# Kernel tuning notes

Measured on AMD Instinct MI355X. Metric: run time of the kernel, lower is better.

## Reference

```python
import jax, jax.numpy as jnp
import numpy as np

INPUT_DIM = 32
HID_DIM = 64
TTCN_DIM = HID_DIM - 1  # 63
N, LX = 128, 512


def setup_inputs() -> dict:
    key = jax.random.key(0)
    ks = jax.random.split(key, 10)
    X_int = jax.random.normal(ks[0], (N, LX, INPUT_DIM), dtype=jnp.float32)
    mask_X = jax.random.randint(ks[1], (N, LX, 1), 0, 2).astype(jnp.float32)
    s1 = 1.0 / np.sqrt(INPUT_DIM)
    s2 = 1.0 / np.sqrt(TTCN_DIM)
    W1 = jax.random.uniform(ks[2], (INPUT_DIM, TTCN_DIM), jnp.float32, -s1, s1)
    b1 = jax.random.uniform(ks[3], (TTCN_DIM,), jnp.float32, -s1, s1)
    W2 = jax.random.uniform(ks[4], (TTCN_DIM, TTCN_DIM), jnp.float32, -s2, s2)
    b2 = jax.random.uniform(ks[5], (TTCN_DIM,), jnp.float32, -s2, s2)
    W3 = jax.random.uniform(ks[6], (TTCN_DIM, INPUT_DIM * TTCN_DIM), jnp.float32, -s2, s2)
    b3 = jax.random.uniform(ks[7], (INPUT_DIM * TTCN_DIM,), jnp.float32, -s2, s2)
    T_bias = jax.random.normal(ks[8], (1, TTCN_DIM), dtype=jnp.float32)
    return {"X_int": X_int, "mask_X": mask_X, "W1": W1, "b1": b1,
            "W2": W2, "b2": b2, "W3": W3, "b3": b3, "T_bias": T_bias}


def reference(X_int, mask_X, W1, b1, W2, b2, W3, b3, T_bias):
    n, lx, d = X_int.shape
    k = TTCN_DIM
    # 3-layer MLP filter generator: (N, Lx, D*K)
    h = jax.nn.relu(X_int @ W1 + b1)
    h = jax.nn.relu(h @ W2 + b2)
    filt = h @ W3 + b3
    # masked softmax over the time axis Lx
    filt = filt * mask_X + (1.0 - mask_X) * (-1e8)
    filt = jax.nn.softmax(filt, axis=1)  # softmax over Lx
    filt = filt.reshape(n, lx, k, d)     # (N, Lx, K, D)
    # attention-weighted pooling: sum over Lx and D
    out = jnp.einsum('nld,nlkd->nk', X_int, filt)
    return jax.nn.relu(out + T_bias)
```

## Files before the change

kernel.cpp:

```cpp
#include <hip/hip_runtime.h>
#include <hip/hip_bf16.h>


#define N_   128
#define LX_  512
#define D_   32
#define K_   63
#define C_   2016
#define LOG2E 1.44269504088896f

typedef __bf16 bf16x8 __attribute__((ext_vector_type(8)));
typedef float floatx4 __attribute__((ext_vector_type(4)));

static __device__ __forceinline__ floatx4 mfma16(bf16x8 a, bf16x8 b, floatx4 c) {
  return __builtin_amdgcn_mfma_f32_16x16x32_bf16(a, b, c, 0, 0, 0);
}

#define HC_OFF   0u
#define XMC_OFF  (8u * 1024u * 1024u)
#define W3FR_OFF (12u * 1024u * 1024u)
#define W1FR_OFF (W3FR_OFF + 258048u)
#define W2FR_OFF (W1FR_OFF + 4096u)
#define B1_OFF   (W2FR_OFF + 8192u)
#define POS_OFF  (B1_OFF + 256u)
#define CNT_OFF  (POS_OFF + 262144u)

__global__ __launch_bounds__(256) void kern_prep(
    const float* __restrict__ Mk,
    const float* __restrict__ W1, const float* __restrict__ b1,
    const float* __restrict__ W2, const float* __restrict__ b2,
    const float* __restrict__ W3, const float* __restrict__ b3,
    __bf16* __restrict__ W3fr, __bf16* __restrict__ W1fr,
    __bf16* __restrict__ W2fr, float* __restrict__ b1pad,
    int* __restrict__ pos, int* __restrict__ cnt,
    __bf16* __restrict__ Hc, __bf16* __restrict__ Xmc) {
  const int n = blockIdx.x, tid = threadIdx.x;
  __shared__ int s_cnt;

  if (tid < 64) {
    const int lane = tid;
    int running = 0;
    for (int c = 0; c < 8; ++c) {
      const int l = c * 64 + lane;
      const float mkv = Mk[n * LX_ + l];
      const unsigned long long b = __ballot(mkv > 0.5f);
      const int mypos = running + __popcll(b & ((1ull << lane) - 1ull));
      pos[n * LX_ + l] = (mkv > 0.5f) ? mypos : -1;
      running += __popcll(b);
    }
    if (lane == 0) { cnt[n] = running; s_cnt = running; }
  }
  __syncthreads();

  const int c0 = s_cnt, c1 = (c0 + 63) & ~63;
  const float4 z = {0.f, 0.f, 0.f, 0.f};
  for (int idx = tid; idx < (c1 - c0) * 12; idx += 256) {
    const int row = c0 + idx / 12, q = idx % 12;
    if (q < 8) *(float4*)(Hc  + ((size_t)(n * 512 + row)) * 64 + q * 8) = z;
    else       *(float4*)(Xmc + ((size_t)(n * 512 + row)) * 32 + (q - 8) * 8) = z;
  }

  for (int g = n * 256 + tid; g < 129024 + 2048 + 4096 + 64; g += N_ * 256) {
    if (g < 129024) {
      const int j = g & 7, quad = (g >> 3) & 3, l16 = (g >> 5) & 15, h = (g >> 9) & 1;
      const int rest = g >> 10, i = rest % 6, tile = rest / 6;
      const int c = tile * 96 + i * 16 + l16;
      const int t = h * 32 + quad * 8 + j;
      W3fr[g] = (__bf16)(((t < K_) ? W3[(size_t)t * C_ + c] : b3[c]) * LOG2E);
    } else if (g < 129024 + 2048) {
      const int g2 = g - 129024;
      const int j = g2 & 7, quad = (g2 >> 3) & 3, l16 = (g2 >> 5) & 15, i = g2 >> 9;
      const int ch = i * 16 + l16, t = quad * 8 + j;
      W1fr[g2] = (__bf16)((ch < K_) ? W1[t * K_ + ch] : 0.f);
    } else if (g < 129024 + 2048 + 4096) {
      const int g2 = g - 129024 - 2048;
      const int j = g2 & 7, quad = (g2 >> 3) & 3, l16 = (g2 >> 5) & 15, h = (g2 >> 9) & 1;
      const int i = g2 >> 10;
      const int ch = i * 16 + l16, t = h * 32 + quad * 8 + j;
      float v;
      if (t < K_) v = (ch < K_) ? W2[t * K_ + ch] : 0.f;
      else        v = (ch < K_) ? b2[ch] : 1.f;
      W2fr[g2] = (__bf16)v;
    } else {
      const int g2 = g - 129024 - 2048 - 4096;
      b1pad[g2] = (g2 < K_) ? b1[g2] : 0.f;
    }
  }
}

__global__ __launch_bounds__(256) void kern_mlp(
    const float* __restrict__ X, const __bf16* __restrict__ W1fr,
    const __bf16* __restrict__ W2fr, const float* __restrict__ b1pad,
    const int* __restrict__ pos, __bf16* __restrict__ Hc,
    __bf16* __restrict__ Xmc) {
  __shared__ float h1s[4][16][68];
  const int tid = threadIdx.x;
  const int w = tid >> 6, lane = tid & 63, quad = lane >> 4, l16 = lane & 15;

  bf16x8 b1f[4], b2f[4][2];
  float b1v[4];
#pragma unroll
  for (int i = 0; i < 4; ++i) {
    b1f[i]    = *(const bf16x8*)(W1fr + ((i * 16 + l16) * 4 + quad) * 8);
    b2f[i][0] = *(const bf16x8*)(W2fr + (((i * 2 + 0) * 16 + l16) * 4 + quad) * 8);
    b2f[i][1] = *(const bf16x8*)(W2fr + (((i * 2 + 1) * 16 + l16) * 4 + quad) * 8);
    b1v[i] = b1pad[i * 16 + l16];
  }

  const int tok0 = blockIdx.x * 64 + w * 16;
  const int n = tok0 >> 9;
  const float* xp = X + (size_t)(tok0 + l16) * D_ + quad * 8;
  const float4 xa = *(const float4*)xp;
  const float4 xb = *(const float4*)(xp + 4);
  bf16x8 a1;
  a1[0]=(__bf16)xa.x; a1[1]=(__bf16)xa.y; a1[2]=(__bf16)xa.z; a1[3]=(__bf16)xa.w;
  a1[4]=(__bf16)xb.x; a1[5]=(__bf16)xb.y; a1[6]=(__bf16)xb.z; a1[7]=(__bf16)xb.w;

  const int px = pos[tok0 + l16];
  int pr[4];
#pragma unroll
  for (int r = 0; r < 4; ++r) pr[r] = pos[tok0 + quad * 4 + r];

  if (px >= 0)
    *(bf16x8*)(Xmc + ((size_t)(n * 512 + px)) * 32 + quad * 8) = a1;

#pragma unroll
  for (int i = 0; i < 4; ++i) {
    floatx4 acc = {0.f, 0.f, 0.f, 0.f};
    acc = mfma16(a1, b1f[i], acc);
#pragma unroll
    for (int r = 0; r < 4; ++r) {
      float v = fmaxf(acc[r] + b1v[i], 0.f);
      if (i == 3 && l16 == 15) v = 1.f;
      h1s[w][quad * 4 + r][i * 16 + l16] = v;
    }
  }

  const float* hrow = &h1s[w][l16][0];
  const float4 p0 = *(const float4*)(hrow + quad * 8);
  const float4 p1 = *(const float4*)(hrow + quad * 8 + 4);
  const float4 p2 = *(const float4*)(hrow + 32 + quad * 8);
  const float4 p3 = *(const float4*)(hrow + 32 + quad * 8 + 4);
  bf16x8 a20, a21;
  a20[0]=(__bf16)p0.x; a20[1]=(__bf16)p0.y; a20[2]=(__bf16)p0.z; a20[3]=(__bf16)p0.w;
  a20[4]=(__bf16)p1.x; a20[5]=(__bf16)p1.y; a20[6]=(__bf16)p1.z; a20[7]=(__bf16)p1.w;
  a21[0]=(__bf16)p2.x; a21[1]=(__bf16)p2.y; a21[2]=(__bf16)p2.z; a21[3]=(__bf16)p2.w;
  a21[4]=(__bf16)p3.x; a21[5]=(__bf16)p3.y; a21[6]=(__bf16)p3.z; a21[7]=(__bf16)p3.w;

#pragma unroll
  for (int i = 0; i < 4; ++i) {
    floatx4 acc = {0.f, 0.f, 0.f, 0.f};
    acc = mfma16(a20, b2f[i][0], acc);
    acc = mfma16(a21, b2f[i][1], acc);
#pragma unroll
    for (int r = 0; r < 4; ++r) {
      if (pr[r] >= 0)
        Hc[((size_t)(n * 512 + pr[r])) * 64 + i * 16 + l16] =
            (__bf16)fmaxf(acc[r], 0.f);
    }
  }
}

__global__ __launch_bounds__(256) void kern_att(
    const __bf16* __restrict__ Hc, const __bf16* __restrict__ Xmc,
    const __bf16* __restrict__ W3fr, const int* __restrict__ cnt,
    const float* __restrict__ Tb, float* __restrict__ out) {
  __shared__ float redS[4][96], redO[4][96];
  __shared__ float rbuf[96];

  const int bid = blockIdx.x;
  const int idx = bid >> 3;
  const int n = (bid & 7) * 16 + idx / 21;
  const int bt = idx % 21;
  const int tid = threadIdx.x;
  const int w = tid >> 6, lane = tid & 63, quad = lane >> 4, l16 = lane & 15;

  bf16x8 bf[6][2];
#pragma unroll
  for (int i = 0; i < 6; ++i) {
    bf[i][0] = *(const bf16x8*)(W3fr + ((((bt * 6 + i) * 2 + 0) * 16 + l16) * 4 + quad) * 8);
    bf[i][1] = *(const bf16x8*)(W3fr + ((((bt * 6 + i) * 2 + 1) * 16 + l16) * 4 + quad) * 8);
  }

  const int cntn = cnt[n];
  const int iters = (cntn + 63) >> 6;
  const __bf16* Hn = Hc + ((size_t)n << 9) * 64;
  const __bf16* Xn = Xmc + ((size_t)n << 9) * 32;

  float s[6] = {0, 0, 0, 0, 0, 0}, o[6] = {0, 0, 0, 0, 0, 0};

  int lw = w * 16;
  bf16x8 a0 = *(const bf16x8*)(Hn + (size_t)(lw + l16) * 64 + quad * 8);
  bf16x8 a1 = *(const bf16x8*)(Hn + (size_t)(lw + l16) * 64 + 32 + quad * 8);
  float xl[4], xh[4];
#pragma unroll
  for (int r = 0; r < 4; ++r) {
    xl[r] = (float)Xn[(lw + quad * 4 + r) * 32 + l16];
    xh[r] = (float)Xn[(lw + quad * 4 + r) * 32 + 16 + l16];
  }

#pragma unroll 1
  for (int it = 0;;) {
    bf16x8 na0, na1;
    float nxl[4], nxh[4];
    const int nlw = lw + 64;
    if (it + 1 < iters) {
      na0 = *(const bf16x8*)(Hn + (size_t)(nlw + l16) * 64 + quad * 8);
      na1 = *(const bf16x8*)(Hn + (size_t)(nlw + l16) * 64 + 32 + quad * 8);
#pragma unroll
      for (int r = 0; r < 4; ++r) {
        nxl[r] = (float)Xn[(nlw + quad * 4 + r) * 32 + l16];
        nxh[r] = (float)Xn[(nlw + quad * 4 + r) * 32 + 16 + l16];
      }
    }

    float v[4];
#pragma unroll
    for (int r = 0; r < 4; ++r) v[r] = (lw + quad * 4 + r < cntn) ? 1.f : 0.f;

#pragma unroll
    for (int i = 0; i < 6; ++i) {
      floatx4 acc = {0.f, 0.f, 0.f, 0.f};
      acc = mfma16(a0, bf[i][0], acc);
      acc = mfma16(a1, bf[i][1], acc);
      const float* xv = (i & 1) ? xh : xl;
#pragma unroll
      for (int r = 0; r < 4; ++r) {
        const float e = __builtin_amdgcn_exp2f(acc[r]);
        s[i] = fmaf(v[r], e, s[i]);
        o[i] = fmaf(e, xv[r], o[i]);
      }
    }

    if (++it >= iters) break;
    lw = nlw;
    a0 = na0; a1 = na1;
#pragma unroll
    for (int r = 0; r < 4; ++r) { xl[r] = nxl[r]; xh[r] = nxh[r]; }
  }

#pragma unroll
  for (int i = 0; i < 6; ++i) {
    s[i] += __shfl_xor(s[i], 16);
    s[i] += __shfl_xor(s[i], 32);
    o[i] += __shfl_xor(o[i], 16);
    o[i] += __shfl_xor(o[i], 32);
  }
  if (quad == 0) {
#pragma unroll
    for (int i = 0; i < 6; ++i) {
      redS[w][i * 16 + l16] = s[i];
      redO[w][i * 16 + l16] = o[i];
    }
  }
  __syncthreads();
  if (tid < 96) {
    const float S = redS[0][tid] + redS[1][tid] + redS[2][tid] + redS[3][tid];
    const float O = redO[0][tid] + redO[1][tid] + redO[2][tid] + redO[3][tid];
    rbuf[tid] = O / S;
  }
  __syncthreads();
  if (tid < 3) {
    float acc = 0.f;
#pragma unroll
    for (int dd = 0; dd < 32; ++dd) acc += rbuf[tid * 32 + dd];
    const int k = bt * 3 + tid;
    out[n * K_ + k] = fmaxf(acc + Tb[k], 0.f);
  }
}

extern "C" void kernel_launch(void* const* d_in, const int* in_sizes, int n_in,
                              void* d_out, int out_size, void* d_ws, size_t ws_size,
                              hipStream_t stream) {
  const float* X  = (const float*)d_in[0];
  const float* Mk = (const float*)d_in[1];
  const float* W1 = (const float*)d_in[2];
  const float* b1 = (const float*)d_in[3];
  const float* W2 = (const float*)d_in[4];
  const float* b2 = (const float*)d_in[5];
  const float* W3 = (const float*)d_in[6];
  const float* b3 = (const float*)d_in[7];
  const float* Tb = (const float*)d_in[8];
  float* out = (float*)d_out;

  char* ws = (char*)d_ws;
  __bf16* Hc    = (__bf16*)(ws + HC_OFF);
  __bf16* Xmc   = (__bf16*)(ws + XMC_OFF);
  __bf16* W3fr  = (__bf16*)(ws + W3FR_OFF);
  __bf16* W1fr  = (__bf16*)(ws + W1FR_OFF);
  __bf16* W2fr  = (__bf16*)(ws + W2FR_OFF);
  float*  b1pad = (float*)(ws + B1_OFF);
  int*    pos   = (int*)(ws + POS_OFF);
  int*    cnt   = (int*)(ws + CNT_OFF);

  kern_prep<<<N_, 256, 0, stream>>>(Mk, W1, b1, W2, b2, W3, b3,
                                    W3fr, W1fr, W2fr, b1pad, pos, cnt, Hc, Xmc);
  kern_mlp<<<N_ * LX_ / 64, 256, 0, stream>>>(X, W1fr, W2fr, b1pad, pos, Hc, Xmc);
  kern_att<<<N_ * 21, 256, 0, stream>>>(Hc, Xmc, W3fr, cnt, Tb, out);
}
```

Baseline: 113.7 us.

## Store compacted X transposed in fp32 chunks and process 16-row chunks in attention

Compacted X is now stored as fp32 in a chunk-transposed layout, so the attention kernel reads it with float4 loads instead of scalar bf16 gathers. The attention loop now steps through 16-row chunks instead of 64-row iterations, which trims wasted padded work. The per-row validity mask is dropped and the padded rows' contribution to the softmax sum is subtracted afterwards. The transposed writes in the MLP kernel become strided scalar stores, and the fp32 buffer doubles the workspace traffic for X.

```diff
diff --git a/kernel.cpp b/kernel.cpp
--- a/kernel.cpp
+++ b/kernel.cpp
@@ -11,14 +11,15 @@
 
 typedef __bf16 bf16x8 __attribute__((ext_vector_type(8)));
 typedef float floatx4 __attribute__((ext_vector_type(4)));
+typedef float floatx2 __attribute__((ext_vector_type(2)));
 
 static __device__ __forceinline__ floatx4 mfma16(bf16x8 a, bf16x8 b, floatx4 c) {
   return __builtin_amdgcn_mfma_f32_16x16x32_bf16(a, b, c, 0, 0, 0);
 }
 
 #define HC_OFF   0u
-#define XMC_OFF  (8u * 1024u * 1024u)
-#define W3FR_OFF (12u * 1024u * 1024u)
+#define XT_OFF   (8u * 1024u * 1024u)
+#define W3FR_OFF (16u * 1024u * 1024u)
 #define W1FR_OFF (W3FR_OFF + 258048u)
 #define W2FR_OFF (W1FR_OFF + 4096u)
 #define B1_OFF   (W2FR_OFF + 8192u)
@@ -33,7 +34,7 @@
     __bf16* __restrict__ W3fr, __bf16* __restrict__ W1fr,
     __bf16* __restrict__ W2fr, float* __restrict__ b1pad,
     int* __restrict__ pos, int* __restrict__ cnt,
-    __bf16* __restrict__ Hc, __bf16* __restrict__ Xmc) {
+    __bf16* __restrict__ Hc, float* __restrict__ Xt) {
   const int n = blockIdx.x, tid = threadIdx.x;
   __shared__ int s_cnt;
 
@@ -54,10 +55,14 @@
 
   const int c0 = s_cnt, c1 = (c0 + 63) & ~63;
   const float4 z = {0.f, 0.f, 0.f, 0.f};
-  for (int idx = tid; idx < (c1 - c0) * 12; idx += 256) {
-    const int row = c0 + idx / 12, q = idx % 12;
-    if (q < 8) *(float4*)(Hc  + ((size_t)(n * 512 + row)) * 64 + q * 8) = z;
-    else       *(float4*)(Xmc + ((size_t)(n * 512 + row)) * 32 + (q - 8) * 8) = z;
+  for (int idx = tid; idx < (c1 - c0) * 40; idx += 256) {
+    const int row = c0 + idx / 40, q = idx % 40;
+    if (q < 8) {
+      *(float4*)(Hc + ((size_t)(n * 512 + row)) * 64 + q * 8) = z;
+    } else {
+      const int d = q - 8;
+      Xt[((size_t)(n * 32 + (row >> 4)) * 32 + d) * 16 + (row & 15)] = 0.f;
+    }
   }
 
   for (int g = n * 256 + tid; g < 129024 + 2048 + 4096 + 64; g += N_ * 256) {
@@ -92,7 +97,7 @@
     const float* __restrict__ X, const __bf16* __restrict__ W1fr,
     const __bf16* __restrict__ W2fr, const float* __restrict__ b1pad,
     const int* __restrict__ pos, __bf16* __restrict__ Hc,
-    __bf16* __restrict__ Xmc) {
+    float* __restrict__ Xt) {
   __shared__ float h1s[4][16][68];
   const int tid = threadIdx.x;
   const int w = tid >> 6, lane = tid & 63, quad = lane >> 4, l16 = lane & 15;
@@ -121,8 +126,12 @@
 #pragma unroll
   for (int r = 0; r < 4; ++r) pr[r] = pos[tok0 + quad * 4 + r];
 
-  if (px >= 0)
-    *(bf16x8*)(Xmc + ((size_t)(n * 512 + px)) * 32 + quad * 8) = a1;
+  if (px >= 0) {
+    float* xtp = Xt + ((size_t)(n * 32 + (px >> 4)) * 32 + quad * 8) * 16 + (px & 15);
+    const float vals[8] = {xa.x, xa.y, xa.z, xa.w, xb.x, xb.y, xb.z, xb.w};
+#pragma unroll
+    for (int j = 0; j < 8; ++j) xtp[j * 16] = vals[j];
+  }
 
 #pragma unroll
   for (int i = 0; i < 4; ++i) {
@@ -162,7 +171,7 @@
 }
 
 __global__ __launch_bounds__(256) void kern_att(
-    const __bf16* __restrict__ Hc, const __bf16* __restrict__ Xmc,
+    const __bf16* __restrict__ Hc, const float* __restrict__ Xt,
     const __bf16* __restrict__ W3fr, const int* __restrict__ cnt,
     const float* __restrict__ Tb, float* __restrict__ out) {
   __shared__ float redS[4][96], redO[4][96];
@@ -183,79 +192,77 @@
   }
 
   const int cntn = cnt[n];
-  const int iters = (cntn + 63) >> 6;
-  const __bf16* Hn = Hc + ((size_t)n << 9) * 64;
-  const __bf16* Xn = Xmc + ((size_t)n << 9) * 32;
-
-  float s[6] = {0, 0, 0, 0, 0, 0}, o[6] = {0, 0, 0, 0, 0, 0};
-
-  int lw = w * 16;
-  bf16x8 a0 = *(const bf16x8*)(Hn + (size_t)(lw + l16) * 64 + quad * 8);
-  bf16x8 a1 = *(const bf16x8*)(Hn + (size_t)(lw + l16) * 64 + 32 + quad * 8);
-  float xl[4], xh[4];
-#pragma unroll
-  for (int r = 0; r < 4; ++r) {
-    xl[r] = (float)Xn[(lw + quad * 4 + r) * 32 + l16];
-    xh[r] = (float)Xn[(lw + quad * 4 + r) * 32 + 16 + l16];
-  }
+  const int nch = (cntn + 15) >> 4;
+  const __bf16* Hb = Hc + ((size_t)n << 9) * 64 + (size_t)l16 * 64 + quad * 8;
+  const float*  Xb = Xt + ((size_t)n * 32) * 512 + l16 * 16 + quad * 4;
+
+  floatx2 s2[3] = {{0.f, 0.f}, {0.f, 0.f}, {0.f, 0.f}};
+  float o[6] = {0, 0, 0, 0, 0, 0};
+
+  int c = w;
+  bf16x8 a0 = *(const bf16x8*)(Hb + (size_t)c * 1024);
+  bf16x8 a1 = *(const bf16x8*)(Hb + (size_t)c * 1024 + 32);
+  float4 xl4 = *(const float4*)(Xb + c * 512);
+  float4 xh4 = *(const float4*)(Xb + c * 512 + 256);
 
 #pragma unroll 1
-  for (int it = 0;;) {
+  while (c < nch) {
+    const int cn = c + 4;
     bf16x8 na0, na1;
-    float nxl[4], nxh[4];
-    const int nlw = lw + 64;
-    if (it + 1 < iters) {
-      na0 = *(const bf16x8*)(Hn + (size_t)(nlw + l16) * 64 + quad * 8);
-      na1 = *(const bf16x8*)(Hn + (size_t)(nlw + l16) * 64 + 32 + quad * 8);
+    float4 nxl, nxh;
+    if (cn < nch) {
+      na0 = *(const bf16x8*)(Hb + (size_t)cn * 1024);
+      na1 = *(const bf16x8*)(Hb + (size_t)cn * 1024 + 32);
+      nxl = *(const float4*)(Xb + cn * 512);
+      nxh = *(const float4*)(Xb + cn * 512 + 256);
+    }
+
+#pragma unroll
+    for (int t = 0; t < 3; ++t) {
+      floatx4 accE = {0.f, 0.f, 0.f, 0.f};
+      floatx4 accO = {0.f, 0.f, 0.f, 0.f};
+      accE = mfma16(a0, bf[2 * t][0], accE);
+      accE = mfma16(a1, bf[2 * t][1], accE);
+      accO = mfma16(a0, bf[2 * t + 1][0], accO);
+      accO = mfma16(a1, bf[2 * t + 1][1], accO);
 #pragma unroll
       for (int r = 0; r < 4; ++r) {
-        nxl[r] = (float)Xn[(nlw + quad * 4 + r) * 32 + l16];
-        nxh[r] = (float)Xn[(nlw + quad * 4 + r) * 32 + 16 + l16];
+        floatx2 e2;
+        e2.x = __builtin_amdgcn_exp2f(accE[r]);
+        e2.y = __builtin_amdgcn_exp2f(accO[r]);
+        s2[t] += e2;
+        o[2 * t]     = fmaf(e2.x, xl4[r], o[2 * t]);
+        o[2 * t + 1] = fmaf(e2.y, xh4[r], o[2 * t + 1]);
       }
     }
 
-    float v[4];
-#pragma unroll
-    for (int r = 0; r < 4; ++r) v[r] = (lw + quad * 4 + r < cntn) ? 1.f : 0.f;
-
-#pragma unroll
-    for (int i = 0; i < 6; ++i) {
-      floatx4 acc = {0.f, 0.f, 0.f, 0.f};
-      acc = mfma16(a0, bf[i][0], acc);
-      acc = mfma16(a1, bf[i][1], acc);
-      const float* xv = (i & 1) ? xh : xl;
-#pragma unroll
-      for (int r = 0; r < 4; ++r) {
-        const float e = __builtin_amdgcn_exp2f(acc[r]);
-        s[i] = fmaf(v[r], e, s[i]);
-        o[i] = fmaf(e, xv[r], o[i]);
-      }
-    }
-
-    if (++it >= iters) break;
-    lw = nlw;
-    a0 = na0; a1 = na1;
-#pragma unroll
-    for (int r = 0; r < 4; ++r) { xl[r] = nxl[r]; xh[r] = nxh[r]; }
-  }
-
+    c = cn;
+    a0 = na0; a1 = na1; xl4 = nxl; xh4 = nxh;
+  }
+
+#pragma unroll
+  for (int t = 0; t < 3; ++t) {
+    s2[t].x += __shfl_xor(s2[t].x, 16); s2[t].x += __shfl_xor(s2[t].x, 32);
+    s2[t].y += __shfl_xor(s2[t].y, 16); s2[t].y += __shfl_xor(s2[t].y, 32);
+  }
 #pragma unroll
   for (int i = 0; i < 6; ++i) {
-    s[i] += __shfl_xor(s[i], 16);
-    s[i] += __shfl_xor(s[i], 32);
     o[i] += __shfl_xor(o[i], 16);
     o[i] += __shfl_xor(o[i], 32);
   }
   if (quad == 0) {
 #pragma unroll
-    for (int i = 0; i < 6; ++i) {
-      redS[w][i * 16 + l16] = s[i];
-      redO[w][i * 16 + l16] = o[i];
-    }
+    for (int t = 0; t < 3; ++t) {
+      redS[w][(2 * t) * 16 + l16]     = s2[t].x;
+      redS[w][(2 * t + 1) * 16 + l16] = s2[t].y;
+    }
+#pragma unroll
+    for (int i = 0; i < 6; ++i) redO[w][i * 16 + l16] = o[i];
   }
   __syncthreads();
   if (tid < 96) {
-    const float S = redS[0][tid] + redS[1][tid] + redS[2][tid] + redS[3][tid];
+    const float pad = (float)(nch * 16 - cntn);
+    const float S = redS[0][tid] + redS[1][tid] + redS[2][tid] + redS[3][tid] - pad;
     const float O = redO[0][tid] + redO[1][tid] + redO[2][tid] + redO[3][tid];
     rbuf[tid] = O / S;
   }
@@ -285,7 +292,7 @@
 
   char* ws = (char*)d_ws;
   __bf16* Hc    = (__bf16*)(ws + HC_OFF);
-  __bf16* Xmc   = (__bf16*)(ws + XMC_OFF);
+  float*  Xt    = (float*)(ws + XT_OFF);
   __bf16* W3fr  = (__bf16*)(ws + W3FR_OFF);
   __bf16* W1fr  = (__bf16*)(ws + W1FR_OFF);
   __bf16* W2fr  = (__bf16*)(ws + W2FR_OFF);
@@ -294,7 +301,7 @@
   int*    cnt   = (int*)(ws + CNT_OFF);
 
   kern_prep<<<N_, 256, 0, stream>>>(Mk, W1, b1, W2, b2, W3, b3,
-                                    W3fr, W1fr, W2fr, b1pad, pos, cnt, Hc, Xmc);
-  kern_mlp<<<N_ * LX_ / 64, 256, 0, stream>>>(X, W1fr, W2fr, b1pad, pos, Hc, Xmc);
-  kern_att<<<N_ * 21, 256, 0, stream>>>(Hc, Xmc, W3fr, cnt, Tb, out);
-}
+                                    W3fr, W1fr, W2fr, b1pad, pos, cnt, Hc, Xt);
+  kern_mlp<<<N_ * LX_ / 64, 256, 0, stream>>>(X, W1fr, W2fr, b1pad, pos, Hc, Xt);
+  kern_att<<<N_ * 21, 256, 0, stream>>>(Hc, Xt, W3fr, cnt, Tb, out);
+}
```

Result: no change. 112.9 us (-0.7%).
